# Performance work log

Measured on AMD Instinct MI355X. Metric: run time of the kernel, lower is better.

The kernel has to match this reference:

```python
import jax, jax.numpy as jnp
import numpy as np

C_IN = 256
C_INT = C_IN // 2  # inter_channels


def _conv1x1(x, w, b):
    # x: [B, Cin, H, W], w: [Cout, Cin], b: [Cout]
    return jnp.einsum('bchw,oc->bohw', x, w) + b[None, :, None, None]


def setup_inputs() -> dict:
    key = jax.random.key(0)
    ks = jax.random.split(key, 9)
    B, H, W = 8, 64, 64
    s_in = 1.0 / np.sqrt(C_IN)
    s_int = 1.0 / np.sqrt(C_INT)
    return {
        'x': jax.random.normal(ks[0], (B, C_IN, H, W), dtype=jnp.float32),
        'g_w': jax.random.normal(ks[1], (C_INT, C_IN), dtype=jnp.float32) * s_in,
        'g_b': jax.random.normal(ks[2], (C_INT,), dtype=jnp.float32) * s_in,
        'theta_w': jax.random.normal(ks[3], (C_INT, C_IN), dtype=jnp.float32) * s_in,
        'theta_b': jax.random.normal(ks[4], (C_INT,), dtype=jnp.float32) * s_in,
        'phi_w': jax.random.normal(ks[5], (C_INT, C_IN), dtype=jnp.float32) * s_in,
        'phi_b': jax.random.normal(ks[6], (C_INT,), dtype=jnp.float32) * s_in,
        'W_w': jax.random.normal(ks[7], (C_IN, C_INT), dtype=jnp.float32) * s_int,
        'W_b': jax.random.normal(ks[8], (C_IN,), dtype=jnp.float32) * s_int,
    }


def reference(x, g_w, g_b, theta_w, theta_b, phi_w, phi_b, W_w, W_b):
    B, C, H, W = x.shape
    N = H * W
    g_x = _conv1x1(x, g_w, g_b).reshape(B, C_INT, N)        # [B, Ci, N]
    theta_x = _conv1x1(x, theta_w, theta_b).reshape(B, C_INT, N)
    phi_x = _conv1x1(x, phi_w, phi_b).reshape(B, C_INT, N)
    # f[b, i, j] = theta[:, i] . phi[:, j]  (no scaling, per original)
    f = jnp.einsum('bci,bcj->bij', theta_x, phi_x)          # [B, N, N]
    f_div_C = jax.nn.softmax(f, axis=-1)
    y = jnp.einsum('bij,bcj->bci', f_div_C, g_x)            # [B, Ci, N]
    y = y.reshape(B, C_INT, H, W)
    y = _conv1x1(y, W_w, W_b)                               # [B, C, H, W]
    return x + y
```

## Files before the change

kernel.cpp:

```cpp
#include <hip/hip_runtime.h>

typedef _Float16 f16;
typedef _Float16 f16x4 __attribute__((ext_vector_type(4)));
typedef _Float16 f16x8 __attribute__((ext_vector_type(8)));
typedef __fp16 h2 __attribute__((ext_vector_type(2)));
typedef float f32x4 __attribute__((ext_vector_type(4)));
typedef float f32x16 __attribute__((ext_vector_type(16)));

#define MFMA16(a, b, c) __builtin_amdgcn_mfma_f32_16x16x32_f16(a, b, c, 0, 0, 0)
#define MFMA32(a, b, c) __builtin_amdgcn_mfma_f32_32x32x16_f16(a, b, c, 0, 0, 0)

#if defined(__has_builtin)
#if __has_builtin(__builtin_amdgcn_fdot2)
#define HAS_FDOT2 1
#endif
#endif

typedef const __attribute__((address_space(1))) void gvoid;
typedef __attribute__((address_space(3))) void lvoid;
#define GLDS16(g, l) __builtin_amdgcn_global_load_lds((gvoid*)(g), (lvoid*)(l), 16, 0, 0)

__global__ __launch_bounds__(256) void wcvt_k(
    const float* __restrict__ tw, const float* __restrict__ pw,
    const float* __restrict__ gw, const float* __restrict__ ww,
    f16* __restrict__ Wall, f16* __restrict__ Wepi) {
  int i = blockIdx.x * 256 + threadIdx.x;
  if (i < 384 * 256) {
    int c = i >> 8, cp = i & 255;
    float v = (c < 128) ? tw[c * 256 + cp]
            : (c < 256) ? pw[(c - 128) * 256 + cp]
                        : gw[(c - 256) * 256 + cp];
    Wall[i] = (f16)v;
  }
  int j = i - 384 * 256;
  if (j >= 0 && j < 256 * 128) Wepi[j] = (f16)ww[j];
}

__global__ __launch_bounds__(256) void proj_k(
    const float* __restrict__ x, const f16* __restrict__ Wall,
    const float* __restrict__ tb, const float* __restrict__ pb,
    const float* __restrict__ gb, f16* __restrict__ Q, f16* __restrict__ K,
    f16* __restrict__ Vt) {
  __shared__ f16 xs[64 * 264];
  __shared__ f16 vs[128 * 65];
  int b = blockIdx.x >> 6, nt = blockIdx.x & 63;
  int nbase = nt * 64;
  int tid = threadIdx.x;

  int nq = tid & 15, kq0 = tid >> 4;
#pragma unroll
  for (int p = 0; p < 4; ++p) {
    int kq = kq0 + 16 * p;
    float4 ld[4];
#pragma unroll
    for (int j = 0; j < 4; ++j)
      ld[j] = *(const float4*)(x + ((size_t)b * 256 + 4 * kq + j) * 4096 + nbase + 4 * nq);
#pragma unroll
    for (int e = 0; e < 4; ++e) {
      f16x4 wv = {(f16)((&ld[0].x)[e]), (f16)((&ld[1].x)[e]), (f16)((&ld[2].x)[e]),
                  (f16)((&ld[3].x)[e])};
      *(f16x4*)(&xs[(4 * nq + e) * 264 + 4 * kq]) = wv;
    }
  }
  __syncthreads();

  int w = tid >> 6, lane = tid & 63;
  int lr = lane & 15, lhi = lane >> 4;
  f16x8 a[8];
#pragma unroll
  for (int ks = 0; ks < 8; ++ks)
    a[ks] = *(const f16x8*)(&xs[(w * 16 + lr) * 264 + ks * 32 + lhi * 8]);
  f32x4 acc[24];
#pragma unroll
  for (int ct = 0; ct < 24; ++ct) {
    acc[ct] = {0.f, 0.f, 0.f, 0.f};
    const f16x8* wr = (const f16x8*)(Wall + (size_t)(ct * 16 + lr) * 256);
#pragma unroll
    for (int ks = 0; ks < 8; ++ks) acc[ct] = MFMA16(a[ks], wr[ks * 4 + lhi], acc[ct]);
  }
  int nloc = w * 16 + lhi * 4;
#pragma unroll
  for (int ct = 0; ct < 24; ++ct) {
    int c = ct * 16 + lr;
    float bias = (c < 128) ? tb[c] : (c < 256) ? pb[c - 128] : gb[c - 256];
#pragma unroll
    for (int r = 0; r < 4; ++r) {
      float v = acc[ct][r] + bias;
      int n = nbase + nloc + r;
      if (c < 128) {
        Q[((size_t)b * 4096 + n) * 128 + c] = (f16)v;
      } else if (c < 256) {
        int d = c - 128;
        int slot = ((d >> 4) << 6) + ((n & 31) << 1) + ((d >> 3) & 1);
        K[(size_t)b * 524288 + (size_t)(n >> 5) * 4096 + slot * 8 + (d & 7)] = (f16)v;
      } else {
        vs[(c - 256) * 65 + nloc + r] = (f16)v;
      }
    }
  }
  __syncthreads();
  f16* vo = Vt + (size_t)b * 524288;
  for (int rep = 0; rep < 32; ++rep) {
    int idx = rep * 256 + tid;
    int c = idx >> 6, j = idx & 63;
    int n = nbase + j;
    int nl = j & 31;
    int p = (nl & 3) | ((nl & 4) << 1) | ((nl & 8) >> 1) | (nl & 16);
    int g = p >> 3, e = p & 7;
    int slot = ((c >> 5) << 7) + ((g >> 1) << 6) + ((c & 31) << 1) + (g & 1);
    vo[(size_t)(n >> 5) * 4096 + slot * 8 + e] = vs[c * 65 + j];
  }
}

__global__ __launch_bounds__(256, 3) void attn_k(const f16* __restrict__ Q,
                                                 const f16* __restrict__ K,
                                                 const f16* __restrict__ Vt,
                                                 f16* __restrict__ Yp,
                                                 float2* __restrict__ ml) {
  __shared__ f16 Ks[2][32 * 128];
  __shared__ f16 Vs[2][128 * 32];
  const float L = 1.44269504f;
  int swzid = ((blockIdx.x & 7) << 7) | ((int)blockIdx.x >> 3);
  int b = swzid >> 7, rem = swzid & 127;
  int qt = rem >> 2, s = rem & 3;
  int qbase = qt * 128;
  int tile0 = s * 32;
  int tid = threadIdx.x;
  int w = tid >> 6, lane = tid & 63;
  int col = lane & 31, hi = lane >> 5;

  const f16* Qr = Q + ((size_t)b * 4096 + qbase + w * 32 + col) * 128;
  f16x8 bq[8];
#pragma unroll
  for (int ks = 0; ks < 8; ++ks) bq[ks] = *(const f16x8*)(Qr + ks * 16 + hi * 8);

  f32x16 yacc[4];
#pragma unroll
  for (int dt = 0; dt < 4; ++dt)
#pragma unroll
    for (int r = 0; r < 16; ++r) yacc[dt][r] = 0.f;
  float lv[4] = {0.f, 0.f, 0.f, 0.f};
  float m = -1e30f, nmL = 1e30f;

  const char* KbB = (const char*)(K + (size_t)b * 524288);
  const char* VbB = (const char*)(Vt + (size_t)b * 524288);
  char* KsB = (char*)&Ks[0][0];
  char* VsB = (char*)&Vs[0][0];

  auto stage = [&](int t, int buf) {
    size_t tb_ = (size_t)(tile0 + t) * 8192;
    const char* kb = KbB + tb_ + w * 2048 + lane * 16;
    const char* vb = VbB + tb_ + w * 2048 + lane * 16;
    char* kl = KsB + buf * 8192 + w * 2048;
    char* vl = VsB + buf * 8192 + w * 2048;
#pragma unroll
    for (int c = 0; c < 2; ++c) {
      GLDS16(kb + c * 1024, kl + c * 1024);
      GLDS16(vb + c * 1024, vl + c * 1024);
    }
  };

  int lanebase = col * 32 + hi * 16;

  stage(0, 0);

  for (int t = 0; t < 32; ++t) {
    int cur = t & 1;
    __syncthreads();
    if (t + 1 < 32) stage(t + 1, cur ^ 1);

    f32x16 s2;
#pragma unroll
    for (int r = 0; r < 16; ++r) s2[r] = 0.f;
    __builtin_amdgcn_s_setprio(1);
    {
      const char* kcur = KsB + cur * 8192 + lanebase;
#pragma unroll
      for (int ks = 0; ks < 8; ++ks) {
        f16x8 ak = *(const f16x8*)(kcur + ks * 1024);
        s2 = MFMA32(ak, bq[ks], s2);
      }
    }
    __builtin_amdgcn_s_setprio(0);

    float a0 = fmaxf(fmaxf(s2[0], s2[1]), s2[2]);
    float a1 = fmaxf(fmaxf(s2[3], s2[4]), s2[5]);
    float a2 = fmaxf(fmaxf(s2[6], s2[7]), s2[8]);
    float a3 = fmaxf(fmaxf(s2[9], s2[10]), s2[11]);
    float a4 = fmaxf(fmaxf(s2[12], s2[13]), s2[14]);
    float pm = fmaxf(fmaxf(fmaxf(a0, a1), fmaxf(a2, a3)), fmaxf(a4, s2[15]));
    pm = fmaxf(pm, __shfl_xor(pm, 32));
    if (pm > m + 8.f) {
      float sc = __expf(m - pm);
      m = pm;
      nmL = -m * L;
#pragma unroll
      for (int i = 0; i < 4; ++i) lv[i] *= sc;
#pragma unroll
      for (int dt = 0; dt < 4; ++dt)
#pragma unroll
        for (int r = 0; r < 16; ++r) yacc[dt][r] *= sc;
    }
#pragma unroll
    for (int r = 0; r < 16; ++r) s2[r] = exp2f(fmaf(s2[r], L, nmL));

    f16x8 pfrA, pfrB;
#pragma unroll
    for (int c = 0; c < 8; ++c) {
      pfrA[c] = (f16)s2[c];
      pfrB[c] = (f16)s2[8 + c];
    }
#if defined(HAS_FDOT2)
    {
      h2 one2 = {1.0f, 1.0f};
      const h2* pa = (const h2*)&pfrA;
      const h2* pb2 = (const h2*)&pfrB;
#pragma unroll
      for (int j = 0; j < 4; ++j) {
        lv[j] = __builtin_amdgcn_fdot2(pa[j], one2, lv[j], false);
        lv[j] = __builtin_amdgcn_fdot2(pb2[j], one2, lv[j], false);
      }
    }
#else
#pragma unroll
    for (int j = 0; j < 4; ++j)
      lv[j] += (float)pfrA[2 * j] + (float)pfrA[2 * j + 1] + (float)pfrB[2 * j] +
               (float)pfrB[2 * j + 1];
#endif

    __builtin_amdgcn_s_setprio(1);
    {
      const char* vcur = VsB + cur * 8192 + lanebase;
#pragma unroll
      for (int dt = 0; dt < 4; ++dt) {
        f16x8 av0 = *(const f16x8*)(vcur + dt * 2048);
        yacc[dt] = MFMA32(av0, pfrA, yacc[dt]);
        f16x8 av1 = *(const f16x8*)(vcur + dt * 2048 + 1024);
        yacc[dt] = MFMA32(av1, pfrB, yacc[dt]);
      }
    }
    __builtin_amdgcn_s_setprio(0);
  }

  float l = (lv[0] + lv[1]) + (lv[2] + lv[3]);
  l += __shfl_xor(l, 32);

  int rowG = b * 4096 + qbase + w * 32 + col;
  f16* yo = Yp + ((size_t)s * 32768 + rowG) * 128;
  float inv = 1.0f / l;
#pragma unroll
  for (int dt = 0; dt < 4; ++dt)
#pragma unroll
    for (int a = 0; a < 4; ++a) {
      f16x4 ov = {(f16)(yacc[dt][4 * a] * inv), (f16)(yacc[dt][4 * a + 1] * inv),
                  (f16)(yacc[dt][4 * a + 2] * inv), (f16)(yacc[dt][4 * a + 3] * inv)};
      *(f16x4*)(yo + dt * 32 + a * 8 + hi * 4) = ov;
    }
  if (hi == 0) ml[s * 32768 + rowG] = make_float2(m, l);
}

__global__ __launch_bounds__(256) void epi_k(const f16* __restrict__ Yp,
                                             const float2* __restrict__ ml,
                                             const f16* __restrict__ Wepi,
                                             const float* __restrict__ Wb,
                                             const float* __restrict__ x,
                                             float* __restrict__ out) {
  int b = blockIdx.x >> 6, nt = blockIdx.x & 63;
  int nbase = nt * 64;
  int w = threadIdx.x >> 6, lane = threadIdx.x & 63;
  int lr = lane & 15, lhi = lane >> 4;
  f16x8 by[4][4];
#pragma unroll
  for (int n4 = 0; n4 < 4; ++n4) {
    int row = b * 4096 + nbase + n4 * 16 + lr;
    float2 m0 = ml[row], m1 = ml[32768 + row], m2 = ml[65536 + row], m3 = ml[98304 + row];
    float mm = fmaxf(fmaxf(m0.x, m1.x), fmaxf(m2.x, m3.x));
    float w0 = m0.y * __expf(m0.x - mm), w1 = m1.y * __expf(m1.x - mm);
    float w2 = m2.y * __expf(m2.x - mm), w3 = m3.y * __expf(m3.x - mm);
    float inv = 1.f / (w0 + w1 + w2 + w3);
    w0 *= inv; w1 *= inv; w2 *= inv; w3 *= inv;
    size_t rb = (size_t)row * 128;
#pragma unroll
    for (int ks = 0; ks < 4; ++ks) {
      int eo = ks * 32 + lhi * 8;
      f16x8 a0 = *(const f16x8*)(Yp + rb + eo);
      f16x8 a1 = *(const f16x8*)(Yp + (size_t)32768 * 128 + rb + eo);
      f16x8 a2 = *(const f16x8*)(Yp + (size_t)65536 * 128 + rb + eo);
      f16x8 a3 = *(const f16x8*)(Yp + (size_t)98304 * 128 + rb + eo);
      f16x8 o;
#pragma unroll
      for (int e = 0; e < 8; ++e)
        o[e] = (f16)(w0 * (float)a0[e] + w1 * (float)a1[e] + w2 * (float)a2[e] +
                     w3 * (float)a3[e]);
      by[n4][ks] = o;
    }
  }
#pragma unroll
  for (int ot = 0; ot < 4; ++ot) {
    int o0 = w * 64 + ot * 16;
    const f16x8* wr = (const f16x8*)(Wepi + (size_t)(o0 + lr) * 128);
    f16x8 a[4];
#pragma unroll
    for (int ks = 0; ks < 4; ++ks) a[ks] = wr[ks * 4 + lhi];
#pragma unroll
    for (int n4 = 0; n4 < 4; ++n4) {
      f32x4 acc = {0.f, 0.f, 0.f, 0.f};
#pragma unroll
      for (int ks = 0; ks < 4; ++ks) acc = MFMA16(a[ks], by[n4][ks], acc);
#pragma unroll
      for (int r = 0; r < 4; ++r) {
        int o = o0 + lhi * 4 + r;
        int n = nbase + n4 * 16 + lr;
        size_t idx = ((size_t)b * 256 + o) * 4096 + n;
        out[idx] = x[idx] + Wb[o] + acc[r];
      }
    }
  }
}

extern "C" void kernel_launch(void* const* d_in, const int* in_sizes, int n_in,
                              void* d_out, int out_size, void* d_ws, size_t ws_size,
                              hipStream_t stream) {
  const float* x       = (const float*)d_in[0];
  const float* g_w     = (const float*)d_in[1];
  const float* g_b     = (const float*)d_in[2];
  const float* theta_w = (const float*)d_in[3];
  const float* theta_b = (const float*)d_in[4];
  const float* phi_w   = (const float*)d_in[5];
  const float* phi_b   = (const float*)d_in[6];
  const float* W_w     = (const float*)d_in[7];
  const float* W_b     = (const float*)d_in[8];
  float* out = (float*)d_out;

  f16* Q    = (f16*)d_ws;
  f16* Kk   = Q + (size_t)8 * 4096 * 128;
  f16* Vt   = Kk + (size_t)8 * 4096 * 128;
  f16* Wall = Vt + (size_t)8 * 4096 * 128;
  f16* Wepi = Wall + 384 * 256;
  float2* ml = (float2*)(Wepi + 256 * 128);
  f16* Yp   = (f16*)(ml + 4 * 32768);

  wcvt_k<<<512, 256, 0, stream>>>(theta_w, phi_w, g_w, W_w, Wall, Wepi);
  proj_k<<<512, 256, 0, stream>>>(x, Wall, theta_b, phi_b, g_b, Q, Kk, Vt);
  attn_k<<<1024, 256, 0, stream>>>(Q, Kk, Vt, Yp, ml);
  epi_k<<<512, 256, 0, stream>>>(Yp, ml, Wepi, W_b, x, out);
}
```

Baseline: 190.5 us.

## Software-pipeline attention with triple-buffered LDS and overlapped QK^T/softmax-PV

Triple-buffers the K/V tiles in LDS and restructures the tile loop into a two-stage software pipeline. Each step computes the QK^T MFMAs for the next tile while running softmax and the PV MFMAs for the previous one. It uses explicit vmcnt waits and raw barriers instead of __syncthreads. The aim is to hide softmax latency and global-load latency behind matrix work, at the cost of more LDS (48KB per block) and an extra score accumulator in registers, which could hurt occupancy or cause spills.

```diff
diff --git a/kernel.cpp b/kernel.cpp
--- a/kernel.cpp
+++ b/kernel.cpp
@@ -19,6 +19,8 @@
 typedef const __attribute__((address_space(1))) void gvoid;
 typedef __attribute__((address_space(3))) void lvoid;
 #define GLDS16(g, l) __builtin_amdgcn_global_load_lds((gvoid*)(g), (lvoid*)(l), 16, 0, 0)
+
+__device__ __forceinline__ int m3(int t) { return t - (t / 3) * 3; }
 
 __global__ __launch_bounds__(256) void wcvt_k(
     const float* __restrict__ tw, const float* __restrict__ pw,
@@ -117,8 +119,8 @@
                                                  const f16* __restrict__ Vt,
                                                  f16* __restrict__ Yp,
                                                  float2* __restrict__ ml) {
-  __shared__ f16 Ks[2][32 * 128];
-  __shared__ f16 Vs[2][128 * 32];
+  __shared__ f16 Ks[3][32 * 128];
+  __shared__ f16 Vs[3][128 * 32];
   const float L = 1.44269504f;
   int swzid = ((blockIdx.x & 7) << 7) | ((int)blockIdx.x >> 3);
   int b = swzid >> 7, rem = swzid & 127;
@@ -162,33 +164,26 @@
 
   int lanebase = col * 32 + hi * 16;
 
-  stage(0, 0);
-
-  for (int t = 0; t < 32; ++t) {
-    int cur = t & 1;
-    __syncthreads();
-    if (t + 1 < 32) stage(t + 1, cur ^ 1);
-
-    f32x16 s2;
-#pragma unroll
-    for (int r = 0; r < 16; ++r) s2[r] = 0.f;
+  auto qkt = [&](int buf, f32x16& sN) {
+    const char* kcur = KsB + buf * 8192 + lanebase;
+#pragma unroll
+    for (int r = 0; r < 16; ++r) sN[r] = 0.f;
     __builtin_amdgcn_s_setprio(1);
-    {
-      const char* kcur = KsB + cur * 8192 + lanebase;
-#pragma unroll
-      for (int ks = 0; ks < 8; ++ks) {
-        f16x8 ak = *(const f16x8*)(kcur + ks * 1024);
-        s2 = MFMA32(ak, bq[ks], s2);
-      }
+#pragma unroll
+    for (int ks = 0; ks < 8; ++ks) {
+      f16x8 ak = *(const f16x8*)(kcur + ks * 1024);
+      sN = MFMA32(ak, bq[ks], sN);
     }
     __builtin_amdgcn_s_setprio(0);
-
-    float a0 = fmaxf(fmaxf(s2[0], s2[1]), s2[2]);
-    float a1 = fmaxf(fmaxf(s2[3], s2[4]), s2[5]);
-    float a2 = fmaxf(fmaxf(s2[6], s2[7]), s2[8]);
-    float a3 = fmaxf(fmaxf(s2[9], s2[10]), s2[11]);
-    float a4 = fmaxf(fmaxf(s2[12], s2[13]), s2[14]);
-    float pm = fmaxf(fmaxf(fmaxf(a0, a1), fmaxf(a2, a3)), fmaxf(a4, s2[15]));
+  };
+
+  auto smpv = [&](int buf, f32x16& sO) {
+    float a0 = fmaxf(fmaxf(sO[0], sO[1]), sO[2]);
+    float a1 = fmaxf(fmaxf(sO[3], sO[4]), sO[5]);
+    float a2 = fmaxf(fmaxf(sO[6], sO[7]), sO[8]);
+    float a3 = fmaxf(fmaxf(sO[9], sO[10]), sO[11]);
+    float a4 = fmaxf(fmaxf(sO[12], sO[13]), sO[14]);
+    float pm = fmaxf(fmaxf(fmaxf(a0, a1), fmaxf(a2, a3)), fmaxf(a4, sO[15]));
     pm = fmaxf(pm, __shfl_xor(pm, 32));
     if (pm > m + 8.f) {
       float sc = __expf(m - pm);
@@ -202,13 +197,13 @@
         for (int r = 0; r < 16; ++r) yacc[dt][r] *= sc;
     }
 #pragma unroll
-    for (int r = 0; r < 16; ++r) s2[r] = exp2f(fmaf(s2[r], L, nmL));
+    for (int r = 0; r < 16; ++r) sO[r] = exp2f(fmaf(sO[r], L, nmL));
 
     f16x8 pfrA, pfrB;
 #pragma unroll
     for (int c = 0; c < 8; ++c) {
-      pfrA[c] = (f16)s2[c];
-      pfrB[c] = (f16)s2[8 + c];
+      pfrA[c] = (f16)sO[c];
+      pfrB[c] = (f16)sO[8 + c];
     }
 #if defined(HAS_FDOT2)
     {
@@ -227,20 +222,49 @@
       lv[j] += (float)pfrA[2 * j] + (float)pfrA[2 * j + 1] + (float)pfrB[2 * j] +
                (float)pfrB[2 * j + 1];
 #endif
-
     __builtin_amdgcn_s_setprio(1);
-    {
-      const char* vcur = VsB + cur * 8192 + lanebase;
-#pragma unroll
-      for (int dt = 0; dt < 4; ++dt) {
-        f16x8 av0 = *(const f16x8*)(vcur + dt * 2048);
-        yacc[dt] = MFMA32(av0, pfrA, yacc[dt]);
-        f16x8 av1 = *(const f16x8*)(vcur + dt * 2048 + 1024);
-        yacc[dt] = MFMA32(av1, pfrB, yacc[dt]);
-      }
+    const char* vcur = VsB + buf * 8192 + lanebase;
+#pragma unroll
+    for (int dt = 0; dt < 4; ++dt) {
+      f16x8 av0 = *(const f16x8*)(vcur + dt * 2048);
+      yacc[dt] = MFMA32(av0, pfrA, yacc[dt]);
+      f16x8 av1 = *(const f16x8*)(vcur + dt * 2048 + 1024);
+      yacc[dt] = MFMA32(av1, pfrB, yacc[dt]);
     }
     __builtin_amdgcn_s_setprio(0);
-  }
+  };
+
+#define PH_WAIT4 asm volatile("s_waitcnt vmcnt(4)" ::: "memory")
+#define PH_WAIT0 asm volatile("s_waitcnt vmcnt(0)" ::: "memory")
+#define BAR __builtin_amdgcn_s_barrier()
+
+  f32x16 sA, sB;
+  stage(0, 0);
+  stage(1, 1);
+  PH_WAIT4;
+  BAR;
+  qkt(0, sA);
+  BAR;
+  stage(2, 2);
+  for (int p = 1; p < 31; p += 2) {
+    PH_WAIT4;
+    BAR;
+    qkt(m3(p), sB);
+    smpv(m3(p - 1), sA);
+    BAR;
+    if (p + 2 < 32) stage(p + 2, m3(p + 2));
+    PH_WAIT4;
+    BAR;
+    qkt(m3(p + 1), sA);
+    smpv(m3(p), sB);
+    BAR;
+    if (p + 3 < 32) stage(p + 3, m3(p + 3));
+  }
+  PH_WAIT0;
+  BAR;
+  qkt(m3(31), sB);
+  smpv(m3(30), sA);
+  smpv(m3(31), sB);
 
   float l = (lv[0] + lv[1]) + (lv[2] + lv[3]);
   l += __shfl_xor(l, 32);
```

After: 189.8 us. Within noise of the previous version (-0.3%).
